# Kernel tuning notes

Hardware: AMD Instinct MI355X
Metric: run time of the kernel (lower is better)

## Reference

```python
import jax, jax.numpy as jnp
import numpy as np

B, N, D_S, D_A = 256, 200000, 96, 32
D = D_S + D_A
TIME_HORIZON = 1000
REWARD_SCALE = 5.0
REWARD_BANDWIDTH = 5.0 * TIME_HORIZON / np.sqrt(D)  # bandwidth_scale * T / sqrt(D)
TARGET_WEIGHT = 1.0 / TIME_HORIZON - 1e-6


def setup_inputs() -> dict:
    key = jax.random.key(0)
    k0, k1, k2, k3, k4 = jax.random.split(key, 5)
    state = jax.random.normal(k0, (B, D_S), jnp.float32)
    action = jax.random.normal(k1, (B, D_A), jnp.float32)
    expert_atoms = jax.random.normal(k2, (N, D), jnp.float32)
    expert_weights = jnp.full((N,), 1.0 / N, dtype=jnp.float32)
    scaler_mean = jax.random.normal(k3, (D,), jnp.float32) * 0.1
    scaler_std = jax.random.uniform(k4, (D,), jnp.float32, 0.5, 1.5)
    return {"state": state, "action": action, "expert_atoms": expert_atoms,
            "expert_weights": expert_weights, "scaler_mean": scaler_mean,
            "scaler_std": scaler_std}


def reference(state, action, expert_atoms, expert_weights, scaler_mean, scaler_std):
    # StandardScaler.transform on both agent atoms and expert atoms
    agent = (jnp.concatenate([state, action], axis=1) - scaler_mean) / scaler_std   # [B, D]
    experts = (expert_atoms - scaler_mean) / scaler_std                             # [N, D]
    # pairwise Euclidean distances via ||a||^2 + ||e||^2 - 2 a.e (avoids [B,N,D])
    a2 = jnp.sum(agent * agent, axis=-1)          # [B]
    e2 = jnp.sum(experts * experts, axis=-1)      # [N]
    d2 = a2[:, None] + e2[None, :] - 2.0 * (agent @ experts.T)  # [B, N]
    dists = jnp.sqrt(jnp.maximum(d2, 1e-12))
    # Greedy argmin weight-matching == consume mass in ascending-distance order:
    # sort + cumulative-weight threshold (single fused pass, no host syncs).
    order = jnp.argsort(dists, axis=1)                                # [B, N]
    d_sorted = jnp.take_along_axis(dists, order, axis=1)              # [B, N]
    w_sorted = expert_weights[order]                                  # [B, N]
    cum_prev = jnp.cumsum(w_sorted, axis=1) - w_sorted                # mass consumed before atom i
    take = jnp.clip(TARGET_WEIGHT - cum_prev, 0.0, w_sorted)          # mass taken from atom i
    cost = jnp.sum(take * d_sorted, axis=1)                           # [B]
    return REWARD_SCALE * jnp.exp(-REWARD_BANDWIDTH * cost)
```

## Files before the change

kernel.cpp:

```cpp
#include <hip/hip_runtime.h>
#include <hip/hip_bf16.h>
#include <hip/hip_fp16.h>

#define BATCH 256
#define NEXP 200000
#define DS 96
#define DA 32
#define DIM 128
#define NCHUNK 32
#define NBLK (NEXP / NCHUNK)
#define SAMPLE_N 16384
#define SAMPLE_STRIDE 12
#define SCHUNK 32
#define SBLK (SAMPLE_N / SCHUNK)
#define SAMPLE_TARGET 64
#define MARGIN_BINS 4
#define TAU_BINS 2048
#define TAU_SCALE 16.0f
#define CAND_MAX 2048
#define STAGE_MAX 512
#define CNT_PAD 16
#define NGROUP 32
#define GSLOTS 128
#define HBINS 512
#define RBW 441.94173824159216

static __device__ __forceinline__ float target_w() { return (float)(1.0 / 1000.0 - 1e-6); }

typedef short short8v __attribute__((ext_vector_type(8)));
typedef float f32x4 __attribute__((ext_vector_type(4)));

#define OFF_EBF   0
#define OFF_E2    51200000
#define OFF_SD2   52000000
#define OFF_ABF   60388608
#define OFF_B2    60454144
#define OFF_THR   60455168
#define OFF_CNT2  60456192
#define OFF_CAND2 60980480
#define WS_NEEDED 65174784

__device__ __forceinline__ unsigned short f2bf(float x) {
    __hip_bfloat16 h = __float2bfloat16(x);
    return __builtin_bit_cast(unsigned short, h);
}

__device__ __forceinline__ void load_lds16(const void* g, void* l) {
    __builtin_amdgcn_global_load_lds(
        (const __attribute__((address_space(1))) unsigned int*)g,
        (__attribute__((address_space(3))) unsigned int*)l, 16, 0, 0);
}

__global__ __launch_bounds__(128) void k_agent(const float* __restrict__ state,
                                               const float* __restrict__ action,
                                               const float* __restrict__ stdv,
                                               unsigned short* __restrict__ agent_bf16,
                                               float* __restrict__ b2,
                                               int* __restrict__ cnt2) {
    int b = blockIdx.x, d = threadIdx.x;
    float raw = (d < DS) ? state[b * DS + d] : action[b * DA + (d - DS)];
    float bb = raw / stdv[d];
    agent_bf16[b * DIM + d] = f2bf(bb);
    if (d < NGROUP) cnt2[(b * NGROUP + d) * CNT_PAD] = 0;
    __shared__ float red[128];
    red[d] = bb * bb;
    __syncthreads();
    for (int s = 64; s > 0; s >>= 1) {
        if (d < s) red[d] += red[d + s];
        __syncthreads();
    }
    if (d == 0) b2[b] = red[0];
}

__global__ __launch_bounds__(256) void k_prep(const float* __restrict__ experts,
                                              const float* __restrict__ stdv,
                                              unsigned short* __restrict__ ebf,
                                              float* __restrict__ e2g) {
    __shared__ float rstdl[DIM];
    __shared__ float sq[64 * 33];
    int t = threadIdx.x, blk = blockIdx.x;
    if (t < DIM) rstdl[t] = 1.0f / stdv[t];
    __syncthreads();
    const float4* e4 = reinterpret_cast<const float4*>(experts) + (size_t)blk * 2048;
    ushort4* o4 = reinterpret_cast<ushort4*>(ebf) + (size_t)blk * 2048;
#pragma unroll
    for (int j = 0; j < 8; ++j) {
        int i4 = t + 256 * j;
        float4 v = e4[i4];
        int al = i4 >> 5, c32 = i4 & 31;
        int dbase = c32 * 4;
        float n0 = v.x * rstdl[dbase + 0];
        float n1 = v.y * rstdl[dbase + 1];
        float n2 = v.z * rstdl[dbase + 2];
        float n3 = v.w * rstdl[dbase + 3];
        sq[al * 33 + c32] = n0 * n0 + n1 * n1 + n2 * n2 + n3 * n3;
        ushort4 h; h.x = f2bf(n0); h.y = f2bf(n1); h.z = f2bf(n2); h.w = f2bf(n3);
        o4[i4] = h;
    }
    __syncthreads();
    if (t < 64) {
        float s = 0.f;
#pragma unroll
        for (int i = 0; i < 32; ++i) s += sq[t * 33 + i];
        e2g[blk * 64 + t] = s;
    }
}

__global__ __launch_bounds__(256) void k_sample(const unsigned short* __restrict__ ebf,
                                                const float* __restrict__ e2g,
                                                const unsigned short* __restrict__ agent_bf16,
                                                const float* __restrict__ b2,
                                                _Float16* __restrict__ sd2) {
    __shared__ unsigned short elds[SCHUNK * DIM];
    __shared__ float e2l[SCHUNK];
    __shared__ float b2l[BATCH];

    int t = threadIdx.x, ci = blockIdx.x;
    int lane = t & 63, wave = t >> 6, quad = lane >> 4, lm = lane & 15;
    b2l[t] = b2[t];
    if (t < SCHUNK) e2l[t] = e2g[SAMPLE_STRIDE * (ci * SCHUNK + t)];

    {
        const char* gebf = (const char*)ebf;
        char* lbase = (char*)elds + wave * 2048;
#pragma unroll
        for (int q = 0; q < 2; ++q) {
            int aloc = wave * 8 + q * 4 + (lane >> 4);
            int atomg = SAMPLE_STRIDE * (ci * SCHUNK + aloc);
            int ch = (lane & 15) ^ (aloc & 15);
            load_lds16(gebf + (size_t)atomg * 256 + ch * 16, lbase + q * 1024);
        }
    }

    short8v afrag[4][4];
#pragma unroll
    for (int mt = 0; mt < 4; ++mt)
#pragma unroll
        for (int kk = 0; kk < 4; ++kk) {
            int row = wave * 64 + mt * 16 + lm;
            const uint4* p = reinterpret_cast<const uint4*>(agent_bf16 + row * DIM + kk * 32 + quad * 8);
            afrag[mt][kk] = __builtin_bit_cast(short8v, *p);
        }
    __syncthreads();

    f32x4 zero4 = {0.f, 0.f, 0.f, 0.f};
    f32x4 acc[4][2];
#pragma unroll
    for (int mt = 0; mt < 4; ++mt)
#pragma unroll
        for (int nt = 0; nt < 2; ++nt) acc[mt][nt] = zero4;
#pragma unroll
    for (int kk = 0; kk < 4; ++kk) {
        short8v bfrag[2];
#pragma unroll
        for (int nt = 0; nt < 2; ++nt) {
            int a = nt * 16 + lm;
            int ch = (kk * 4 + quad) ^ (a & 15);
            const uint4* p = reinterpret_cast<const uint4*>((const char*)elds + a * 256 + ch * 16);
            bfrag[nt] = __builtin_bit_cast(short8v, *p);
        }
#pragma unroll
        for (int mt = 0; mt < 4; ++mt)
#pragma unroll
            for (int nt = 0; nt < 2; ++nt)
                acc[mt][nt] = __builtin_amdgcn_mfma_f32_16x16x32_bf16(afrag[mt][kk], bfrag[nt], acc[mt][nt], 0, 0, 0);
    }

#pragma unroll
    for (int mt = 0; mt < 4; ++mt)
#pragma unroll
        for (int nt = 0; nt < 2; ++nt) {
            int atoml = nt * 16 + lm;
            float e2v = e2l[atoml];
#pragma unroll
            for (int r = 0; r < 4; ++r) {
                int row = wave * 64 + mt * 16 + quad * 4 + r;
                float d2 = b2l[row] + fmaf(-2.0f, acc[mt][nt][r], e2v);
                sd2[(size_t)row * SAMPLE_N + ci * SCHUNK + atoml] = (_Float16)d2;
            }
        }
}

__global__ __launch_bounds__(256) void k_tau(const _Float16* __restrict__ sd2,
                                             const float* __restrict__ b2,
                                             float* __restrict__ thr) {
    __shared__ unsigned int hist[TAU_BINS];
    __shared__ unsigned int part[256];
    int t = threadIdx.x, row = blockIdx.x;
    for (int i = t; i < TAU_BINS; i += 256) hist[i] = 0;
    __syncthreads();
    const uint4* r4 = reinterpret_cast<const uint4*>(sd2 + (size_t)row * SAMPLE_N);
#pragma unroll
    for (int it = 0; it < 8; ++it) {
        uint4 v = r4[t + 256 * it];
        unsigned int wv[4] = {v.x, v.y, v.z, v.w};
#pragma unroll
        for (int q = 0; q < 4; ++q)
#pragma unroll
            for (int hh = 0; hh < 2; ++hh) {
                unsigned short bits = (unsigned short)((wv[q] >> (16 * hh)) & 0xffffu);
                float d2f = (float)__builtin_bit_cast(_Float16, bits);
                int bn = (int)(sqrtf(fmaxf(d2f, 0.f)) * TAU_SCALE);
                bn = bn < 0 ? 0 : (bn > TAU_BINS - 1 ? TAU_BINS - 1 : bn);
                atomicAdd(&hist[bn], 1u);
            }
    }
    __syncthreads();
    unsigned int s = 0;
#pragma unroll
    for (int i = 0; i < 8; ++i) s += hist[t * 8 + i];
    part[t] = s;
    __syncthreads();
    if (t == 0) {
        unsigned int cum = 0;
        int B = TAU_BINS - 1;
        for (int c = 0; c < 256; ++c) {
            if (cum + part[c] >= SAMPLE_TARGET) {
                unsigned int cc = cum;
                for (int i = 0; i < 8; ++i) {
                    cc += hist[c * 8 + i];
                    if (cc >= SAMPLE_TARGET) { B = c * 8 + i; break; }
                }
                break;
            }
            cum += part[c];
        }
        int tb = B + MARGIN_BINS;
        if (tb > TAU_BINS - 1) tb = TAU_BINS - 1;
        float td = (float)(tb + 1) * (1.0f / TAU_SCALE);
        thr[row] = td * td - b2[row];
    }
}

__global__ __launch_bounds__(256, 4) void k_compact(const unsigned short* __restrict__ ebf,
                                                    const float* __restrict__ e2g,
                                                    const unsigned short* __restrict__ agent_bf16,
                                                    const float* __restrict__ thr,
                                                    const float* __restrict__ b2,
                                                    int* __restrict__ cnt2,
                                                    float* __restrict__ cand2) {
    __shared__ unsigned short elds[NCHUNK * DIM];
    __shared__ float e2l[NCHUNK];
    __shared__ float thrl[BATCH], b2l[BATCH];
    __shared__ unsigned int stage_pk[STAGE_MAX];
    __shared__ float stage_d2[STAGE_MAX];
    __shared__ int rowcnt[BATCH], rowbase[BATCH], rowoff[BATCH];
    __shared__ int nlds;

    int t = threadIdx.x, chunkblk = blockIdx.x;
    int grp = chunkblk % NGROUP;
    int lane = t & 63, wave = t >> 6, quad = lane >> 4, lm = lane & 15;
    thrl[t] = thr[t];
    b2l[t] = b2[t];
    if (t < NCHUNK) e2l[t] = e2g[chunkblk * NCHUNK + t];
    rowcnt[t] = 0; rowoff[t] = 0;
    if (t == 0) nlds = 0;

    {
        const char* gbase = (const char*)ebf + (size_t)chunkblk * NCHUNK * 256;
        char* lbase = (char*)elds + wave * 2048;
#pragma unroll
        for (int q = 0; q < 2; ++q) {
            int aloc = wave * 8 + q * 4 + (lane >> 4);
            int ch = (lane & 15) ^ (aloc & 15);
            load_lds16(gbase + (size_t)aloc * 256 + ch * 16, lbase + q * 1024);
        }
    }
    __syncthreads();

    f32x4 zero4 = {0.f, 0.f, 0.f, 0.f};
    f32x4 acc[4][2];
#pragma unroll
    for (int mt = 0; mt < 4; ++mt)
#pragma unroll
        for (int nt = 0; nt < 2; ++nt) acc[mt][nt] = zero4;

#pragma unroll
    for (int kk = 0; kk < 4; ++kk) {
        short8v afrag[4];
#pragma unroll
        for (int mt = 0; mt < 4; ++mt) {
            int row = wave * 64 + mt * 16 + lm;
            const uint4* p = reinterpret_cast<const uint4*>(agent_bf16 + row * DIM + kk * 32 + quad * 8);
            afrag[mt] = __builtin_bit_cast(short8v, *p);
        }
#pragma unroll
        for (int nt = 0; nt < 2; ++nt) {
            int a = nt * 16 + lm;
            int ch = (kk * 4 + quad) ^ (a & 15);
            const uint4* p = reinterpret_cast<const uint4*>((const char*)elds + a * 256 + ch * 16);
            short8v bfrag = __builtin_bit_cast(short8v, *p);
#pragma unroll
            for (int mt = 0; mt < 4; ++mt)
                acc[mt][nt] = __builtin_amdgcn_mfma_f32_16x16x32_bf16(afrag[mt], bfrag, acc[mt][nt], 0, 0, 0);
        }
    }

#pragma unroll
    for (int mt = 0; mt < 4; ++mt)
#pragma unroll
        for (int nt = 0; nt < 2; ++nt) {
            int atoml = nt * 16 + lm;
            float e2v = e2l[atoml];
#pragma unroll
            for (int r = 0; r < 4; ++r) {
                int row = wave * 64 + mt * 16 + quad * 4 + r;
                float lhs = fmaf(-2.0f, acc[mt][nt][r], e2v);
                if (lhs <= thrl[row]) {
                    int p = atomicAdd(&nlds, 1);
                    if (p < STAGE_MAX) {
                        stage_pk[p] = (unsigned int)row;
                        stage_d2[p] = b2l[row] + lhs;
                        atomicAdd(&rowcnt[row], 1);
                    }
                }
            }
        }
    __syncthreads();
    int n = nlds < STAGE_MAX ? nlds : STAGE_MAX;

    int rc = rowcnt[t];
    if (rc > 0) rowbase[t] = atomicAdd(&cnt2[(t * NGROUP + grp) * CNT_PAD], rc);
    __syncthreads();

    for (int i = t; i < n; i += 256) {
        int row = (int)(stage_pk[i] & 255u);
        int pos = rowbase[row] + atomicAdd(&rowoff[row], 1);
        if (pos < GSLOTS) cand2[(row * NGROUP + grp) * GSLOTS + pos] = stage_d2[i];
    }
}

__global__ __launch_bounds__(256) void k_cost(const float* __restrict__ cand2,
                                              const int* __restrict__ cnt2,
                                              const float* __restrict__ weights,
                                              const float* __restrict__ thr,
                                              const float* __restrict__ b2,
                                              float* __restrict__ out) {
    __shared__ float cdl[CAND_MAX];
    __shared__ unsigned int hist[HBINS];
    __shared__ unsigned int part[256];
    __shared__ int gcnt[NGROUP], goff[NGROUP + 1];
    __shared__ float bb[64];
    __shared__ float wred[4];
    __shared__ unsigned int wtot[4];
    __shared__ int nb;
    __shared__ int Bs, c0s;
    __shared__ float dmin2S;

    int t = threadIdx.x, row = blockIdx.x;
    int lane = t & 63, wave = t >> 6;
    for (int i = t; i < HBINS; i += 256) hist[i] = 0;
    if (t < NGROUP) {
        int nn = cnt2[(row * NGROUP + t) * CNT_PAD];
        gcnt[t] = nn < GSLOTS ? nn : GSLOTS;
    }
    if (t == 0) nb = 0;
    __syncthreads();
    if (t == 0) {
        int s = 0;
        for (int g = 0; g < NGROUP; ++g) { goff[g] = s; s += gcnt[g]; }
        goff[NGROUP] = s < CAND_MAX ? s : CAND_MAX;
    }
    __syncthreads();
    int nc = goff[NGROUP];
    float tau2 = thr[row] + b2[row];

    {
        for (int g = wave; g < NGROUP; g += 4) {
            int n = gcnt[g], base = goff[g];
            const float* src = cand2 + (row * NGROUP + g) * GSLOTS;
            for (int i = lane; i < n; i += 64) {
                int slot = base + i;
                if (slot < CAND_MAX) cdl[slot] = src[i];
            }
        }
    }
    __syncthreads();

    float mn = tau2;
    for (int i = t; i < nc; i += 256) mn = fminf(mn, cdl[i]);
#pragma unroll
    for (int o = 32; o >= 1; o >>= 1) mn = fminf(mn, __shfl_xor(mn, o, 64));
    if (lane == 0) wred[wave] = mn;
    __syncthreads();
    if (t == 0) dmin2S = fminf(fminf(wred[0], wred[1]), fminf(wred[2], wred[3]));
    __syncthreads();
    float dmin2 = dmin2S;
    float denom = tau2 - dmin2;
    float binscale = (float)HBINS / fmaxf(denom, 1e-12f);

    for (int i = t; i < nc; i += 256) {
        int bn = (int)((cdl[i] - dmin2) * binscale);
        bn = bn < 0 ? 0 : (bn > HBINS - 1 ? HBINS - 1 : bn);
        atomicAdd(&hist[bn], 1u);
    }
    __syncthreads();

    unsigned int pv = hist[2 * t] + hist[2 * t + 1];
    part[t] = pv;
    unsigned int inc = pv;
#pragma unroll
    for (int o = 1; o < 64; o <<= 1) {
        unsigned int up = __shfl_up(inc, o, 64);
        if (lane >= o) inc += up;
    }
    if (lane == 63) wtot[wave] = inc;
    __syncthreads();
    unsigned int woffs = 0;
    for (int w = 0; w < wave; ++w) woffs += wtot[w];
    unsigned int incl = inc + woffs;
    unsigned int before = incl - pv;
    if (before < 200u && incl >= 200u) {
        unsigned int h0 = hist[2 * t];
        if (before + h0 >= 200u) { Bs = 2 * t; c0s = (int)before; }
        else { Bs = 2 * t + 1; c0s = (int)(before + h0); }
    }
    __syncthreads();
    int B = Bs, c0 = c0s;

    float sloc = 0.f;
    for (int i = t; i < nc; i += 256) {
        float d2 = cdl[i];
        int bn = (int)((d2 - dmin2) * binscale);
        bn = bn < 0 ? 0 : (bn > HBINS - 1 ? HBINS - 1 : bn);
        if (bn < B) sloc += sqrtf(fmaxf(d2, 1e-12f));
        else if (bn == B) {
            int p = atomicAdd(&nb, 1);
            if (p < 64) bb[p] = sqrtf(fmaxf(d2, 1e-12f));
        }
    }
#pragma unroll
    for (int o = 32; o >= 1; o >>= 1) sloc += __shfl_xor(sloc, o, 64);
    if (lane == 0) wred[wave] = sloc;
    __syncthreads();

    if (t == 0) {
        float s0 = wred[0] + wred[1] + wred[2] + wred[3];
        int m = nb < 64 ? nb : 64;
        for (int i = 1; i < m; ++i) {
            float v = bb[i]; int j = i - 1;
            while (j >= 0 && bb[j] > v) { bb[j + 1] = bb[j]; --j; }
            bb[j + 1] = v;
        }
        int need = 200 - c0;
        if (need > m) need = m;
        float s199 = s0;
        for (int i = 0; i < need - 1; ++i) s199 += bb[i];
        float d200 = bb[need - 1];
        float w0 = weights[0];
        float cumw = 0.f;
        for (int i = 0; i < 199; ++i) cumw += w0;
        float TGT = target_w();
        float cost = w0 * s199 + (TGT - cumw) * d200;
        out[row] = 5.0f * expf(-(float)RBW * cost);
    }
}

extern "C" void kernel_launch(void* const* d_in, const int* in_sizes, int n_in,
                              void* d_out, int out_size, void* d_ws, size_t ws_size,
                              hipStream_t stream) {
    const float* state   = (const float*)d_in[0];
    const float* action  = (const float*)d_in[1];
    const float* experts = (const float*)d_in[2];
    const float* weights = (const float*)d_in[3];
    const float* stdv    = (const float*)d_in[5];
    float* out = (float*)d_out;

    if (ws_size < (size_t)WS_NEEDED) return;

    char* ws = (char*)d_ws;
    unsigned short* ebf        = (unsigned short*)(ws + OFF_EBF);
    float* e2g                 = (float*)(ws + OFF_E2);
    _Float16* sd2              = (_Float16*)(ws + OFF_SD2);
    unsigned short* agent_bf16 = (unsigned short*)(ws + OFF_ABF);
    float* b2                  = (float*)(ws + OFF_B2);
    float* thr                 = (float*)(ws + OFF_THR);
    int* cnt2                  = (int*)(ws + OFF_CNT2);
    float* cand2               = (float*)(ws + OFF_CAND2);

    k_agent<<<BATCH, 128, 0, stream>>>(state, action, stdv, agent_bf16, b2, cnt2);
    k_prep<<<NBLK / 2, 256, 0, stream>>>(experts, stdv, ebf, e2g);
    k_sample<<<SBLK, 256, 0, stream>>>(ebf, e2g, agent_bf16, b2, sd2);
    k_tau<<<BATCH, 256, 0, stream>>>(sd2, b2, thr);
    k_compact<<<NBLK, 256, 0, stream>>>(ebf, e2g, agent_bf16, thr, b2, cnt2, cand2);
    k_cost<<<BATCH, 256, 0, stream>>>(cand2, cnt2, weights, thr, b2, out);
}
```

Measured before the change: 258.4 us.

## Fuse agent prep into expert prep and double-buffer two chunks per compact block

Folds the agent normalization, squared norm and counter reset into the first blocks of the expert prep kernel, removing a separate launch. The compact kernel now handles two expert chunks per block, prefetching the second chunk into LDS while the first is being scored, and shares staging and global atomics across both. This halves the compact grid and per-block setup, but with more atoms per block the fixed-size staging buffer is more likely to overflow.

After: 254.0 us. Within noise of the previous version (-1.7%).

```diff
diff --git a/kernel.cpp b/kernel.cpp
--- a/kernel.cpp
+++ b/kernel.cpp
@@ -8,7 +8,9 @@
 #define DA 32
 #define DIM 128
 #define NCHUNK 32
-#define NBLK (NEXP / NCHUNK)
+#define CPB 2
+#define CGRID (NEXP / (NCHUNK * CPB))
+#define PREP_BLK 3125
 #define SAMPLE_N 16384
 #define SAMPLE_STRIDE 12
 #define SCHUNK 32
@@ -51,34 +53,19 @@
         (__attribute__((address_space(3))) unsigned int*)l, 16, 0, 0);
 }
 
-__global__ __launch_bounds__(128) void k_agent(const float* __restrict__ state,
-                                               const float* __restrict__ action,
-                                               const float* __restrict__ stdv,
-                                               unsigned short* __restrict__ agent_bf16,
-                                               float* __restrict__ b2,
-                                               int* __restrict__ cnt2) {
-    int b = blockIdx.x, d = threadIdx.x;
-    float raw = (d < DS) ? state[b * DS + d] : action[b * DA + (d - DS)];
-    float bb = raw / stdv[d];
-    agent_bf16[b * DIM + d] = f2bf(bb);
-    if (d < NGROUP) cnt2[(b * NGROUP + d) * CNT_PAD] = 0;
-    __shared__ float red[128];
-    red[d] = bb * bb;
-    __syncthreads();
-    for (int s = 64; s > 0; s >>= 1) {
-        if (d < s) red[d] += red[d + s];
-        __syncthreads();
-    }
-    if (d == 0) b2[b] = red[0];
-}
-
 __global__ __launch_bounds__(256) void k_prep(const float* __restrict__ experts,
                                               const float* __restrict__ stdv,
+                                              const float* __restrict__ state,
+                                              const float* __restrict__ action,
                                               unsigned short* __restrict__ ebf,
-                                              float* __restrict__ e2g) {
+                                              float* __restrict__ e2g,
+                                              unsigned short* __restrict__ agent_bf16,
+                                              float* __restrict__ b2,
+                                              int* __restrict__ cnt2) {
     __shared__ float rstdl[DIM];
     __shared__ float sq[64 * 33];
     int t = threadIdx.x, blk = blockIdx.x;
+    int lane = t & 63, wave = t >> 6;
     if (t < DIM) rstdl[t] = 1.0f / stdv[t];
     __syncthreads();
     const float4* e4 = reinterpret_cast<const float4*>(experts) + (size_t)blk * 2048;
@@ -104,6 +91,22 @@
         for (int i = 0; i < 32; ++i) s += sq[t * 33 + i];
         e2g[blk * 64 + t] = s;
     }
+    if (blk < BATCH) {
+        __syncthreads();
+        float rbb = 0.f;
+        if (t < DIM) {
+            float raw = (t < DS) ? state[blk * DS + t] : action[blk * DA + (t - DS)];
+            float bb = raw * rstdl[t];
+            agent_bf16[blk * DIM + t] = f2bf(bb);
+            rbb = bb * bb;
+        }
+        if (t < NGROUP) cnt2[(blk * NGROUP + t) * CNT_PAD] = 0;
+#pragma unroll
+        for (int o = 32; o >= 1; o >>= 1) rbb += __shfl_xor(rbb, o, 64);
+        if (lane == 0) sq[wave] = rbb;
+        __syncthreads();
+        if (t == 0) b2[blk] = sq[0] + sq[1] + sq[2] + sq[3];
+    }
 }
 
 __global__ __launch_bounds__(256) void k_sample(const unsigned short* __restrict__ ebf,
@@ -239,26 +242,26 @@
                                                     const float* __restrict__ b2,
                                                     int* __restrict__ cnt2,
                                                     float* __restrict__ cand2) {
-    __shared__ unsigned short elds[NCHUNK * DIM];
-    __shared__ float e2l[NCHUNK];
+    __shared__ unsigned short elds[CPB][NCHUNK * DIM];
+    __shared__ float e2l[CPB][NCHUNK];
     __shared__ float thrl[BATCH], b2l[BATCH];
     __shared__ unsigned int stage_pk[STAGE_MAX];
     __shared__ float stage_d2[STAGE_MAX];
     __shared__ int rowcnt[BATCH], rowbase[BATCH], rowoff[BATCH];
     __shared__ int nlds;
 
-    int t = threadIdx.x, chunkblk = blockIdx.x;
-    int grp = chunkblk % NGROUP;
+    int t = threadIdx.x, blk = blockIdx.x;
+    int grp = blk % NGROUP;
     int lane = t & 63, wave = t >> 6, quad = lane >> 4, lm = lane & 15;
     thrl[t] = thr[t];
     b2l[t] = b2[t];
-    if (t < NCHUNK) e2l[t] = e2g[chunkblk * NCHUNK + t];
+    if (t < NCHUNK) e2l[0][t] = e2g[(blk * CPB) * NCHUNK + t];
     rowcnt[t] = 0; rowoff[t] = 0;
     if (t == 0) nlds = 0;
 
     {
-        const char* gbase = (const char*)ebf + (size_t)chunkblk * NCHUNK * 256;
-        char* lbase = (char*)elds + wave * 2048;
+        const char* gbase = (const char*)ebf + (size_t)(blk * CPB) * NCHUNK * 256;
+        char* lbase = (char*)elds[0] + wave * 2048;
 #pragma unroll
         for (int q = 0; q < 2; ++q) {
             int aloc = wave * 8 + q * 4 + (lane >> 4);
@@ -268,55 +271,73 @@
     }
     __syncthreads();
 
-    f32x4 zero4 = {0.f, 0.f, 0.f, 0.f};
-    f32x4 acc[4][2];
-#pragma unroll
-    for (int mt = 0; mt < 4; ++mt)
-#pragma unroll
-        for (int nt = 0; nt < 2; ++nt) acc[mt][nt] = zero4;
-
-#pragma unroll
-    for (int kk = 0; kk < 4; ++kk) {
-        short8v afrag[4];
-#pragma unroll
-        for (int mt = 0; mt < 4; ++mt) {
-            int row = wave * 64 + mt * 16 + lm;
-            const uint4* p = reinterpret_cast<const uint4*>(agent_bf16 + row * DIM + kk * 32 + quad * 8);
-            afrag[mt] = __builtin_bit_cast(short8v, *p);
-        }
-#pragma unroll
-        for (int nt = 0; nt < 2; ++nt) {
-            int a = nt * 16 + lm;
-            int ch = (kk * 4 + quad) ^ (a & 15);
-            const uint4* p = reinterpret_cast<const uint4*>((const char*)elds + a * 256 + ch * 16);
-            short8v bfrag = __builtin_bit_cast(short8v, *p);
-#pragma unroll
-            for (int mt = 0; mt < 4; ++mt)
-                acc[mt][nt] = __builtin_amdgcn_mfma_f32_16x16x32_bf16(afrag[mt], bfrag, acc[mt][nt], 0, 0, 0);
-        }
-    }
-
-#pragma unroll
-    for (int mt = 0; mt < 4; ++mt)
-#pragma unroll
-        for (int nt = 0; nt < 2; ++nt) {
-            int atoml = nt * 16 + lm;
-            float e2v = e2l[atoml];
-#pragma unroll
-            for (int r = 0; r < 4; ++r) {
-                int row = wave * 64 + mt * 16 + quad * 4 + r;
-                float lhs = fmaf(-2.0f, acc[mt][nt][r], e2v);
-                if (lhs <= thrl[row]) {
-                    int p = atomicAdd(&nlds, 1);
-                    if (p < STAGE_MAX) {
-                        stage_pk[p] = (unsigned int)row;
-                        stage_d2[p] = b2l[row] + lhs;
-                        atomicAdd(&rowcnt[row], 1);
+#pragma unroll
+    for (int c = 0; c < CPB; ++c) {
+        if (c + 1 < CPB) {
+            int nk = blk * CPB + c + 1;
+            const char* gbase = (const char*)ebf + (size_t)nk * NCHUNK * 256;
+            char* lbase = (char*)elds[c + 1] + wave * 2048;
+#pragma unroll
+            for (int q = 0; q < 2; ++q) {
+                int aloc = wave * 8 + q * 4 + (lane >> 4);
+                int ch = (lane & 15) ^ (aloc & 15);
+                load_lds16(gbase + (size_t)aloc * 256 + ch * 16, lbase + q * 1024);
+            }
+            if (t < NCHUNK) e2l[c + 1][t] = e2g[nk * NCHUNK + t];
+        }
+
+        f32x4 zero4 = {0.f, 0.f, 0.f, 0.f};
+        f32x4 acc[4][2];
+#pragma unroll
+        for (int mt = 0; mt < 4; ++mt)
+#pragma unroll
+            for (int nt = 0; nt < 2; ++nt) acc[mt][nt] = zero4;
+
+#pragma unroll
+        for (int kk = 0; kk < 4; ++kk) {
+            short8v afrag[4];
+#pragma unroll
+            for (int mt = 0; mt < 4; ++mt) {
+                int row = wave * 64 + mt * 16 + lm;
+                const uint4* p = reinterpret_cast<const uint4*>(agent_bf16 + row * DIM + kk * 32 + quad * 8);
+                afrag[mt] = __builtin_bit_cast(short8v, *p);
+            }
+#pragma unroll
+            for (int nt = 0; nt < 2; ++nt) {
+                int a = nt * 16 + lm;
+                int ch = (kk * 4 + quad) ^ (a & 15);
+                const uint4* p = reinterpret_cast<const uint4*>((const char*)elds[c] + a * 256 + ch * 16);
+                short8v bfrag = __builtin_bit_cast(short8v, *p);
+#pragma unroll
+                for (int mt = 0; mt < 4; ++mt)
+                    acc[mt][nt] = __builtin_amdgcn_mfma_f32_16x16x32_bf16(afrag[mt], bfrag, acc[mt][nt], 0, 0, 0);
+            }
+        }
+
+#pragma unroll
+        for (int mt = 0; mt < 4; ++mt)
+#pragma unroll
+            for (int nt = 0; nt < 2; ++nt) {
+                int atoml = nt * 16 + lm;
+                float e2v = e2l[c][atoml];
+#pragma unroll
+                for (int r = 0; r < 4; ++r) {
+                    int row = wave * 64 + mt * 16 + quad * 4 + r;
+                    float lhs = fmaf(-2.0f, acc[mt][nt][r], e2v);
+                    if (lhs <= thrl[row]) {
+                        int p = atomicAdd(&nlds, 1);
+                        if (p < STAGE_MAX) {
+                            stage_pk[p] = (unsigned int)row;
+                            stage_d2[p] = b2l[row] + lhs;
+                            atomicAdd(&rowcnt[row], 1);
+                        }
                     }
                 }
             }
-        }
-    __syncthreads();
+
+        __syncthreads();
+    }
+
     int n = nlds < STAGE_MAX ? nlds : STAGE_MAX;
 
     int rc = rowcnt[t];
@@ -478,10 +499,9 @@
     int* cnt2                  = (int*)(ws + OFF_CNT2);
     float* cand2               = (float*)(ws + OFF_CAND2);
 
-    k_agent<<<BATCH, 128, 0, stream>>>(state, action, stdv, agent_bf16, b2, cnt2);
-    k_prep<<<NBLK / 2, 256, 0, stream>>>(experts, stdv, ebf, e2g);
+    k_prep<<<PREP_BLK, 256, 0, stream>>>(experts, stdv, state, action, ebf, e2g, agent_bf16, b2, cnt2);
     k_sample<<<SBLK, 256, 0, stream>>>(ebf, e2g, agent_bf16, b2, sd2);
     k_tau<<<BATCH, 256, 0, stream>>>(sd2, b2, thr);
-    k_compact<<<NBLK, 256, 0, stream>>>(ebf, e2g, agent_bf16, thr, b2, cnt2, cand2);
+    k_compact<<<CGRID, 256, 0, stream>>>(ebf, e2g, agent_bf16, thr, b2, cnt2, cand2);
     k_cost<<<BATCH, 256, 0, stream>>>(cand2, cnt2, weights, thr, b2, out);
 }
```
